# Optimization experiments

Hardware: AMD Instinct MI355X
Metric: run time of the kernel (lower is better)

## Reference

```python
import jax, jax.numpy as jnp
import numpy as np

NUM_EMBEDDINGS = 1024
EMBEDDING_DIM = 128
COMMITMENT_COST = 0.25


def setup_inputs() -> dict:
    key = jax.random.key(0)
    k1, k2 = jax.random.split(key)
    z = jax.random.normal(k1, (16, EMBEDDING_DIM, 64, 64), dtype=jnp.float32)
    # torch init: uniform(-1/num_embeddings, 1/num_embeddings)
    lim = 1.0 / NUM_EMBEDDINGS
    embedding = jax.random.uniform(
        k2, (NUM_EMBEDDINGS, EMBEDDING_DIM), dtype=jnp.float32,
        minval=-lim, maxval=lim)
    return {"z": z, "embedding": embedding}


def reference(z, embedding):
    b, c, h, w = z.shape  # c == EMBEDDING_DIM
    # (b, h, w, c) -> (b*h*w, c)
    z_flat = jnp.transpose(z, (0, 2, 3, 1)).reshape(-1, c)
    # squared euclidean distances: ||z||^2 + ||e||^2 - 2 z e^T  -> (N, K)
    distances = (jnp.sum(z_flat ** 2, axis=-1, keepdims=True)
                 + jnp.sum(embedding ** 2, axis=-1)[None, :]
                 - 2.0 * jnp.matmul(z_flat, embedding.T))
    encoding_indices = jnp.argmin(distances, axis=-1)  # (N,) int
    z_q = embedding[encoding_indices].reshape(b, h, w, c)
    z_q = jnp.transpose(z_q, (0, 3, 1, 2))  # (b, c, h, w)
    commitment_loss = COMMITMENT_COST * jnp.sum(
        (jax.lax.stop_gradient(z_q) - z) ** 2)
    codebook_loss = jnp.sum((z_q - jax.lax.stop_gradient(z)) ** 2)
    loss = codebook_loss + commitment_loss
    # straight-through estimator
    z_q_st = z + jax.lax.stop_gradient(z_q - z)
    return (z_q_st, loss, encoding_indices, commitment_loss, codebook_loss)
```

## Files before the change

kernel.cpp:

```cpp
#include <hip/hip_runtime.h>
#include <hip/hip_bf16.h>

#define C 128
#define HW 4096
#define NPOS 65536
#define K 1024
#define MB 128
#define NBLK (NPOS/MB)
#define RS 136
#define RSB 320
#define CHK 64
#define NCH (K/CHK)
#define CHB (CHK*RSB)
#define NRM_OFF 327680

#define ZQ_OFF 0
#define LOSS_OFF 8388608
#define IDX_OFF 8388609
#define COMMIT_OFF 8454145
#define CODE_OFF 8454146

#define WS_IMG_OFF 8192

#define ZT_PAD 9728

typedef __bf16 bf16x8 __attribute__((ext_vector_type(8)));
typedef float f32x4 __attribute__((ext_vector_type(4)));
typedef unsigned short u16x8 __attribute__((ext_vector_type(8)));

__global__ void vq_prep(const float* __restrict__ emb, unsigned char* __restrict__ img,
                        float* __restrict__ S) {
    int k = blockIdx.x;
    int l = threadIdx.x;
    if (k == 0 && l == 0) S[0] = 0.0f;
    float v0 = emb[k * C + l];
    float v1 = emb[k * C + 64 + l];
    __hip_bfloat16 h0 = __float2bfloat16(v0);
    __hip_bfloat16 h1 = __float2bfloat16(v1);
    unsigned short* row = (unsigned short*)(img + (size_t)k * RSB);
    row[l] = *(unsigned short*)&h0;
    row[64 + l] = *(unsigned short*)&h1;
    float s = v0 * v0 + v1 * v1;
    #pragma unroll
    for (int off = 32; off; off >>= 1) s += __shfl_down(s, off);
    if (l == 0) *(float*)(img + NRM_OFF + (size_t)k * 4) = s + 1.0f;
}

__global__ __launch_bounds__(256)
void vq_main(const float* __restrict__ z, const float* __restrict__ emb,
             const unsigned char* __restrict__ img,
             float* __restrict__ out, float* __restrict__ S) {
    __shared__ __align__(16) unsigned short zt[MB * RS + ZT_PAD];
    __shared__ __align__(16) float norm_lds[K];
    __shared__ unsigned int wbest[2][MB];
    __shared__ unsigned short idxs[MB];
    __shared__ float lred[4];

    const int t = threadIdx.x;
    const int w = t >> 6;
    const int lane = t & 63;
    const int nn = lane & 15;
    const int q = lane >> 4;
    const int wm = w >> 1;
    const int wn = w & 1;

    const int blk = blockIdx.x;
    const int n0g = blk * MB;
    const int b = n0g >> 12;
    const int hw0 = n0g & (HW - 1);
    const float* zg = z + (size_t)b * C * HW + hw0;

    __builtin_amdgcn_global_load_lds(
        (const __attribute__((address_space(1))) unsigned int*)(img + NRM_OFF + w * 1024 + lane * 16),
        (__attribute__((address_space(3))) unsigned int*)((unsigned char*)norm_lds + w * 1024),
        16, 0, 0);

    {
        const int pos4 = (t & 31) * 4;
        const int c0 = (t >> 5) * 16;
        float4 fv[16];
        #pragma unroll
        for (int i = 0; i < 16; ++i)
            fv[i] = *(const float4*)&zg[(size_t)(c0 + i) * HW + pos4];
        #pragma unroll
        for (int j = 0; j < 4; ++j) {
            u16x8 p0, p1;
            #pragma unroll
            for (int i = 0; i < 8; ++i) {
                float f0 = (j == 0) ? fv[i].x : (j == 1) ? fv[i].y
                         : (j == 2) ? fv[i].z : fv[i].w;
                float f1 = (j == 0) ? fv[8 + i].x : (j == 1) ? fv[8 + i].y
                         : (j == 2) ? fv[8 + i].z : fv[8 + i].w;
                __hip_bfloat16 h0 = __float2bfloat16(f0);
                __hip_bfloat16 h1 = __float2bfloat16(f1);
                p0[i] = *(unsigned short*)&h0;
                p1[i] = *(unsigned short*)&h1;
            }
            *(u16x8*)&zt[(pos4 + j) * RS + c0] = p0;
            *(u16x8*)&zt[(pos4 + j) * RS + c0 + 8] = p1;
        }
    }
    __syncthreads();

    bf16x8 a[4][4];
    #pragma unroll
    for (int mt = 0; mt < 4; ++mt)
        #pragma unroll
        for (int ks = 0; ks < 4; ++ks) {
            a[mt][ks] = *(bf16x8*)&zt[(wm * 64 + mt * 16 + nn) * RS + ks * 32 + q * 8];
            asm volatile("" : "+v"(*(f32x4*)&a[mt][ks]));
        }

    unsigned int best[4][4];
    #pragma unroll
    for (int mt = 0; mt < 4; ++mt)
        #pragma unroll
        for (int r = 0; r < 4; ++r) best[mt][r] = 0xFFFFFFFFu;

    const unsigned char* pb0 = img + (size_t)(wn * 32 + nn) * RSB + q * 16;
    const unsigned char* pb1 = pb0 + (size_t)16 * RSB;

    bf16x8 b0[4], b1[4];
    #pragma unroll
    for (int ks = 0; ks < 4; ++ks) {
        b0[ks] = *(const bf16x8*)(pb0 + ks * 64);
        b1[ks] = *(const bf16x8*)(pb1 + ks * 64);
    }

    for (int ch = 0; ch < NCH; ++ch) {
        const int step = (ch + 1 < NCH) ? CHB : 0;
        bf16x8 n0[4], n1[4];
        #pragma unroll
        for (int ks = 0; ks < 4; ++ks) {
            n0[ks] = *(const bf16x8*)(pb0 + step + ks * 64);
            n1[ks] = *(const bf16x8*)(pb1 + step + ks * 64);
        }
        const float en0 = norm_lds[ch * CHK + wn * 32 + nn];
        const float en1 = norm_lds[ch * CHK + wn * 32 + 16 + nn];
        const unsigned int code0 = (unsigned int)(ch * CHK + wn * 32 + nn);

        f32x4 acc0[4], acc1[4];
        #pragma unroll
        for (int mt = 0; mt < 4; ++mt) {
            acc0[mt] = (f32x4){0.f, 0.f, 0.f, 0.f};
            acc1[mt] = (f32x4){0.f, 0.f, 0.f, 0.f};
        }
        #pragma unroll
        for (int ks = 0; ks < 4; ++ks)
            #pragma unroll
            for (int mt = 0; mt < 4; ++mt) {
                acc0[mt] = __builtin_amdgcn_mfma_f32_16x16x32_bf16(a[mt][ks], b0[ks], acc0[mt], 0, 0, 0);
                acc1[mt] = __builtin_amdgcn_mfma_f32_16x16x32_bf16(a[mt][ks], b1[ks], acc1[mt], 0, 0, 0);
            }

        #pragma unroll
        for (int mt = 0; mt < 4; ++mt)
            #pragma unroll
            for (int r = 0; r < 4; ++r) {
                float s0 = fmaf(acc0[mt][r], -2.0f, en0);
                float s1 = fmaf(acc1[mt][r], -2.0f, en1);
                unsigned int u0 = (__float_as_uint(s0) & ~1023u) | code0;
                unsigned int u1 = (__float_as_uint(s1) & ~1023u) | (code0 + 16u);
                best[mt][r] = min(best[mt][r], min(u0, u1));
            }

        #pragma unroll
        for (int ks = 0; ks < 4; ++ks) { b0[ks] = n0[ks]; b1[ks] = n1[ks]; }
        pb0 += CHB; pb1 += CHB;
    }

    #pragma unroll
    for (int mt = 0; mt < 4; ++mt)
        #pragma unroll
        for (int r = 0; r < 4; ++r) {
            unsigned int v = best[mt][r];
            v = min(v, (unsigned int)__shfl_xor((int)v, 1));
            v = min(v, (unsigned int)__shfl_xor((int)v, 2));
            v = min(v, (unsigned int)__shfl_xor((int)v, 4));
            v = min(v, (unsigned int)__shfl_xor((int)v, 8));
            if (nn == 0) wbest[wn][wm * 64 + mt * 16 + q * 4 + r] = v;
        }
    __syncthreads();

    if (t < MB) {
        unsigned int v = min(wbest[0][t], wbest[1][t]);
        unsigned int code = v & 1023u;
        idxs[t] = (unsigned short)code;
        out[IDX_OFF + n0g + t] = (float)code;
    }
    __syncthreads();

    {
        const int pos4 = (t & 31) * 4;
        const int c0 = (t >> 5) * 16;
        float* og = out + ZQ_OFF + (size_t)b * C * HW + hw0;
        float ev[4][16];
        float ls = 0.f;
        #pragma unroll
        for (int j = 0; j < 4; ++j) {
            const int pos = pos4 + j;
            const float* erow = emb + (size_t)idxs[pos] * C;
            #pragma unroll
            for (int g = 0; g < 4; ++g) {
                float4 e = *(const float4*)&erow[c0 + g * 4];
                ev[j][g * 4 + 0] = e.x; ev[j][g * 4 + 1] = e.y;
                ev[j][g * 4 + 2] = e.z; ev[j][g * 4 + 3] = e.w;
            }
            u16x8 z0 = *(u16x8*)&zt[pos * RS + c0];
            u16x8 z1 = *(u16x8*)&zt[pos * RS + c0 + 8];
            #pragma unroll
            for (int i = 0; i < 8; ++i) {
                float zf0 = __uint_as_float((unsigned int)z0[i] << 16);
                float zf1 = __uint_as_float((unsigned int)z1[i] << 16);
                float d0 = zf0 - ev[j][i];
                float d1 = zf1 - ev[j][8 + i];
                ls += d0 * d0 + d1 * d1;
            }
        }
        #pragma unroll
        for (int i = 0; i < 16; ++i) {
            float4 v = { ev[0][i], ev[1][i], ev[2][i], ev[3][i] };
            *(float4*)&og[(size_t)(c0 + i) * HW + pos4] = v;
        }
        #pragma unroll
        for (int off = 32; off; off >>= 1) ls += __shfl_down(ls, off);
        if (lane == 0) lred[w] = ls;
    }
    __syncthreads();
    if (t == 0) atomicAdd(S, lred[0] + lred[1] + lred[2] + lred[3]);
}

__global__ void vq_final(const float* __restrict__ S, float* __restrict__ out) {
    float s = *S;
    out[LOSS_OFF] = 1.25f * s;
    out[COMMIT_OFF] = 0.25f * s;
    out[CODE_OFF] = s;
}

extern "C" void kernel_launch(void* const* d_in, const int* in_sizes, int n_in,
                              void* d_out, int out_size, void* d_ws, size_t ws_size,
                              hipStream_t stream) {
    const float* z = (const float*)d_in[0];
    const float* emb = (const float*)d_in[1];
    float* out = (float*)d_out;
    float* S = (float*)d_ws;
    unsigned char* img = (unsigned char*)d_ws + WS_IMG_OFF;

    vq_prep<<<K, 64, 0, stream>>>(emb, img, S);
    vq_main<<<NBLK, 256, 0, stream>>>(z, emb, img, out, S);
    vq_final<<<1, 1, 0, stream>>>(S, out);
}
```

Measured before the change: 113.9 us.

## Stage codebook chunks in LDS with double-buffered async loads and larger blocks

Result: slower. 118.5 us (+4.1%).

```diff
diff --git a/kernel.cpp b/kernel.cpp
--- a/kernel.cpp
+++ b/kernel.cpp
@@ -5,14 +5,13 @@
 #define HW 4096
 #define NPOS 65536
 #define K 1024
-#define MB 128
+#define MB 256
 #define NBLK (NPOS/MB)
 #define RS 136
-#define RSB 320
+#define RSB 272
 #define CHK 64
 #define NCH (K/CHK)
 #define CHB (CHK*RSB)
-#define NRM_OFF 327680
 
 #define ZQ_OFF 0
 #define LOSS_OFF 8388608
@@ -21,8 +20,6 @@
 #define CODE_OFF 8454146
 
 #define WS_IMG_OFF 8192
-
-#define ZT_PAD 9728
 
 typedef __bf16 bf16x8 __attribute__((ext_vector_type(8)));
 typedef float f32x4 __attribute__((ext_vector_type(4)));
@@ -43,18 +40,18 @@
     float s = v0 * v0 + v1 * v1;
     #pragma unroll
     for (int off = 32; off; off >>= 1) s += __shfl_down(s, off);
-    if (l == 0) *(float*)(img + NRM_OFF + (size_t)k * 4) = s + 1.0f;
-}
-
-__global__ __launch_bounds__(256)
+    if (l == 0) *(float*)(img + (size_t)k * RSB + 256) = s + 1.0f;
+}
+
+__global__ __launch_bounds__(512)
 void vq_main(const float* __restrict__ z, const float* __restrict__ emb,
              const unsigned char* __restrict__ img,
              float* __restrict__ out, float* __restrict__ S) {
-    __shared__ __align__(16) unsigned short zt[MB * RS + ZT_PAD];
-    __shared__ __align__(16) float norm_lds[K];
+    __shared__ __align__(16) unsigned short zt[MB * RS];
+    __shared__ __align__(16) unsigned short bbuf[2][CHK * RS];
     __shared__ unsigned int wbest[2][MB];
     __shared__ unsigned short idxs[MB];
-    __shared__ float lred[4];
+    __shared__ float lred[8];
 
     const int t = threadIdx.x;
     const int w = t >> 6;
@@ -69,15 +66,18 @@
     const int b = n0g >> 12;
     const int hw0 = n0g & (HW - 1);
     const float* zg = z + (size_t)b * C * HW + hw0;
-
-    __builtin_amdgcn_global_load_lds(
-        (const __attribute__((address_space(1))) unsigned int*)(img + NRM_OFF + w * 1024 + lane * 16),
-        (__attribute__((address_space(3))) unsigned int*)((unsigned char*)norm_lds + w * 1024),
-        16, 0, 0);
+    unsigned char* ztb = (unsigned char*)zt;
+
+    for (int j = w; j < 17; j += 8) {
+        __builtin_amdgcn_global_load_lds(
+            (const __attribute__((address_space(1))) unsigned int*)(img + j * 1024 + lane * 16),
+            (__attribute__((address_space(3))) unsigned int*)((unsigned char*)bbuf[0] + j * 1024),
+            16, 0, 0);
+    }
 
     {
-        const int pos4 = (t & 31) * 4;
-        const int c0 = (t >> 5) * 16;
+        const int pos4 = (t & 63) * 4;
+        const int c0 = (t >> 6) * 16;
         float4 fv[16];
         #pragma unroll
         for (int i = 0; i < 16; ++i)
@@ -96,8 +96,11 @@
                 p0[i] = *(unsigned short*)&h0;
                 p1[i] = *(unsigned short*)&h1;
             }
-            *(u16x8*)&zt[(pos4 + j) * RS + c0] = p0;
-            *(u16x8*)&zt[(pos4 + j) * RS + c0 + 8] = p1;
+            const unsigned int row = pos4 + j;
+            const unsigned int sw = ((row >> 2) & 7u) << 4;
+            const unsigned int base = row * RSB + c0 * 2;
+            *(u16x8*)(ztb + (base ^ sw)) = p0;
+            *(u16x8*)(ztb + ((base + 16) ^ sw)) = p1;
         }
     }
     __syncthreads();
@@ -107,7 +110,9 @@
     for (int mt = 0; mt < 4; ++mt)
         #pragma unroll
         for (int ks = 0; ks < 4; ++ks) {
-            a[mt][ks] = *(bf16x8*)&zt[(wm * 64 + mt * 16 + nn) * RS + ks * 32 + q * 8];
+            const unsigned int row = wm * 64 + mt * 16 + nn;
+            const unsigned int sw = ((row >> 2) & 7u) << 4;
+            a[mt][ks] = *(bf16x8*)(ztb + ((row * RSB + ks * 64 + q * 16) ^ sw));
             asm volatile("" : "+v"(*(f32x4*)&a[mt][ks]));
         }
 
@@ -117,26 +122,29 @@
         #pragma unroll
         for (int r = 0; r < 4; ++r) best[mt][r] = 0xFFFFFFFFu;
 
-    const unsigned char* pb0 = img + (size_t)(wn * 32 + nn) * RSB + q * 16;
-    const unsigned char* pb1 = pb0 + (size_t)16 * RSB;
-
-    bf16x8 b0[4], b1[4];
-    #pragma unroll
-    for (int ks = 0; ks < 4; ++ks) {
-        b0[ks] = *(const bf16x8*)(pb0 + ks * 64);
-        b1[ks] = *(const bf16x8*)(pb1 + ks * 64);
-    }
-
     for (int ch = 0; ch < NCH; ++ch) {
-        const int step = (ch + 1 < NCH) ? CHB : 0;
-        bf16x8 n0[4], n1[4];
+        const int p = ch & 1;
+        if (ch + 1 < NCH) {
+            const unsigned char* src = img + (size_t)(ch + 1) * CHB;
+            for (int j = w; j < 17; j += 8) {
+                __builtin_amdgcn_global_load_lds(
+                    (const __attribute__((address_space(1))) unsigned int*)(src + j * 1024 + lane * 16),
+                    (__attribute__((address_space(3))) unsigned int*)((unsigned char*)bbuf[p ^ 1] + j * 1024),
+                    16, 0, 0);
+            }
+        }
+        const unsigned short* bb = bbuf[p];
+
+        const int row0 = wn * 32 + nn;
+        const int row1 = row0 + 16;
+        bf16x8 bf0[4], bf1[4];
         #pragma unroll
         for (int ks = 0; ks < 4; ++ks) {
-            n0[ks] = *(const bf16x8*)(pb0 + step + ks * 64);
-            n1[ks] = *(const bf16x8*)(pb1 + step + ks * 64);
-        }
-        const float en0 = norm_lds[ch * CHK + wn * 32 + nn];
-        const float en1 = norm_lds[ch * CHK + wn * 32 + 16 + nn];
+            bf0[ks] = *(const bf16x8*)&bb[row0 * RS + ks * 32 + q * 8];
+            bf1[ks] = *(const bf16x8*)&bb[row1 * RS + ks * 32 + q * 8];
+        }
+        const float en0 = *(const float*)&bb[row0 * RS + 128];
+        const float en1 = *(const float*)&bb[row1 * RS + 128];
         const unsigned int code0 = (unsigned int)(ch * CHK + wn * 32 + nn);
 
         f32x4 acc0[4], acc1[4];
@@ -149,8 +157,8 @@
         for (int ks = 0; ks < 4; ++ks)
             #pragma unroll
             for (int mt = 0; mt < 4; ++mt) {
-                acc0[mt] = __builtin_amdgcn_mfma_f32_16x16x32_bf16(a[mt][ks], b0[ks], acc0[mt], 0, 0, 0);
-                acc1[mt] = __builtin_amdgcn_mfma_f32_16x16x32_bf16(a[mt][ks], b1[ks], acc1[mt], 0, 0, 0);
+                acc0[mt] = __builtin_amdgcn_mfma_f32_16x16x32_bf16(a[mt][ks], bf0[ks], acc0[mt], 0, 0, 0);
+                acc1[mt] = __builtin_amdgcn_mfma_f32_16x16x32_bf16(a[mt][ks], bf1[ks], acc1[mt], 0, 0, 0);
             }
 
         #pragma unroll
@@ -163,10 +171,7 @@
                 unsigned int u1 = (__float_as_uint(s1) & ~1023u) | (code0 + 16u);
                 best[mt][r] = min(best[mt][r], min(u0, u1));
             }
-
-        #pragma unroll
-        for (int ks = 0; ks < 4; ++ks) { b0[ks] = n0[ks]; b1[ks] = n1[ks]; }
-        pb0 += CHB; pb1 += CHB;
+        __syncthreads();
     }
 
     #pragma unroll
@@ -191,8 +196,8 @@
     __syncthreads();
 
     {
-        const int pos4 = (t & 31) * 4;
-        const int c0 = (t >> 5) * 16;
+        const int pos4 = (t & 63) * 4;
+        const int c0 = (t >> 6) * 16;
         float* og = out + ZQ_OFF + (size_t)b * C * HW + hw0;
         float ev[4][16];
         float ls = 0.f;
@@ -206,8 +211,11 @@
                 ev[j][g * 4 + 0] = e.x; ev[j][g * 4 + 1] = e.y;
                 ev[j][g * 4 + 2] = e.z; ev[j][g * 4 + 3] = e.w;
             }
-            u16x8 z0 = *(u16x8*)&zt[pos * RS + c0];
-            u16x8 z1 = *(u16x8*)&zt[pos * RS + c0 + 8];
+            const unsigned int row = (unsigned int)pos;
+            const unsigned int sw = ((row >> 2) & 7u) << 4;
+            const unsigned int base = row * RSB + c0 * 2;
+            u16x8 z0 = *(u16x8*)(ztb + (base ^ sw));
+            u16x8 z1 = *(u16x8*)(ztb + ((base + 16) ^ sw));
             #pragma unroll
             for (int i = 0; i < 8; ++i) {
                 float zf0 = __uint_as_float((unsigned int)z0[i] << 16);
@@ -227,7 +235,12 @@
         if (lane == 0) lred[w] = ls;
     }
     __syncthreads();
-    if (t == 0) atomicAdd(S, lred[0] + lred[1] + lred[2] + lred[3]);
+    if (t == 0) {
+        float bs = 0.f;
+        #pragma unroll
+        for (int i = 0; i < 8; ++i) bs += lred[i];
+        atomicAdd(S, bs);
+    }
 }
 
 __global__ void vq_final(const float* __restrict__ S, float* __restrict__ out) {
@@ -247,6 +260,6 @@
     unsigned char* img = (unsigned char*)d_ws + WS_IMG_OFF;
 
     vq_prep<<<K, 64, 0, stream>>>(emb, img, S);
-    vq_main<<<NBLK, 256, 0, stream>>>(z, emb, img, out, S);
+    vq_main<<<NBLK, 512, 0, stream>>>(z, emb, img, out, S);
     vq_final<<<1, 1, 0, stream>>>(S, out);
 }
```
